# Kernel tuning notes

Measured on AMD Instinct MI355X. Metric: run time of the kernel, lower is better.

## Reference

```python
import jax, jax.numpy as jnp
import numpy as np

N, E = 50000, 800000
F_IN, F_HID, F_OUT = 128, 128, 64


def sage_conv(x, src, dst, Wl, bl, Wr, n_nodes):
    # gather source features, scatter-mean to destination nodes
    msg = x[src]                                                # [E, F]
    agg = jax.ops.segment_sum(msg, dst, num_segments=n_nodes)   # [N, F]
    cnt = jax.ops.segment_sum(jnp.ones((src.shape[0], 1), x.dtype), dst,
                              num_segments=n_nodes)             # [N, 1]
    agg = agg / jnp.maximum(cnt, 1.0)                           # mean; isolated nodes -> 0
    return agg @ Wl + bl + x @ Wr


def setup_inputs() -> dict:
    key = jax.random.key(0)
    ks = jax.random.split(key, 12)
    x = jax.random.normal(ks[0], (N, F_IN), dtype=jnp.float32)
    edge_index = jax.random.randint(ks[1], (2, E), 0, N, dtype=jnp.int64)

    def glorot(k, shape):
        lim = float(np.sqrt(6.0 / (shape[0] + shape[1])))
        return jax.random.uniform(k, shape, jnp.float32, -lim, lim)

    dims = [(F_IN, F_HID), (F_HID, F_HID), (F_HID, F_OUT)]
    params = {}
    for i, (fi, fo) in enumerate(dims):
        params[f"Wl{i}"] = glorot(ks[2 + 3 * i], (fi, fo))
        params[f"bl{i}"] = jnp.zeros((fo,), jnp.float32)
        params[f"Wr{i}"] = glorot(ks[3 + 3 * i], (fi, fo))
    return {"x": x, "edge_index": edge_index, **params}


def reference(x, edge_index, Wl0, bl0, Wr0, Wl1, bl1, Wr1, Wl2, bl2, Wr2):
    src, dst = edge_index[0], edge_index[1]
    layers = [(Wl0, bl0, Wr0), (Wl1, bl1, Wr1), (Wl2, bl2, Wr2)]
    h = x
    for i, (Wl, bl, Wr) in enumerate(layers):
        h = sage_conv(h, src, dst, Wl, bl, Wr, N)
        if i < len(layers) - 1:
            h = jax.nn.elu(h)  # dropout is identity in eval mode
    return jax.nn.log_softmax(h, axis=1)
```

## Files before the change

kernel.cpp:

```cpp
#include <hip/hip_runtime.h>
#include <hip/hip_bf16.h>

#define NN 50000
#define NE 800000
#define NPAD 50048
#define NBK 512
#define RNG 98
#define BCAP 2560
#define CSTRIDE 16
#define EPB 4096
#define NFB ((NE + EPB - 1) / EPB)
#define GB (NPAD / 64)
#define GB2 (NPAD / 32)
#define CSRCAP2 768

typedef __attribute__((ext_vector_type(8))) short bf8;
typedef __attribute__((ext_vector_type(4))) float f4;
typedef __attribute__((ext_vector_type(2))) float f2v;
typedef __attribute__((ext_vector_type(4))) unsigned int u4v;
typedef __attribute__((ext_vector_type(2))) unsigned int u2v;

__device__ __forceinline__ unsigned short f2bf(float f) {
    union { float f; unsigned int u; } x; x.f = f;
    unsigned int r = x.u + 0x7fffu + ((x.u >> 16) & 1u);
    return (unsigned short)(r >> 16);
}
__device__ __forceinline__ float b2f(short s) {
    union { unsigned int u; float f; } x;
    x.u = ((unsigned int)(unsigned short)s) << 16;
    return x.f;
}
__device__ __forceinline__ unsigned char f2fp8(float v) {
    return (unsigned char)(__builtin_amdgcn_cvt_pk_fp8_f32(v, v, 0, false) & 0xff);
}
__device__ __forceinline__ void acc16_fp8(float* acc, u4v v) {
    #pragma unroll
    for (int t = 0; t < 4; ++t) {
        f2v lo = __builtin_amdgcn_cvt_pk_f32_fp8((int)v[t], false);
        f2v hi = __builtin_amdgcn_cvt_pk_f32_fp8((int)v[t], true);
        acc[t * 4 + 0] += lo.x; acc[t * 4 + 1] += lo.y;
        acc[t * 4 + 2] += hi.x; acc[t * 4 + 3] += hi.y;
    }
}
__device__ __forceinline__ void acc8_fp8(float* acc, u2v v) {
    #pragma unroll
    for (int t = 0; t < 2; ++t) {
        f2v lo = __builtin_amdgcn_cvt_pk_f32_fp8((int)v[t], false);
        f2v hi = __builtin_amdgcn_cvt_pk_f32_fp8((int)v[t], true);
        acc[t * 4 + 0] += lo.x; acc[t * 4 + 1] += lo.y;
        acc[t * 4 + 2] += hi.x; acc[t * 4 + 3] += hi.y;
    }
}

__global__ void zero_k(int* __restrict__ cursor, int* __restrict__ rowptr) {
    cursor[threadIdx.x * CSTRIDE] = 0;
    if (threadIdx.x == 0) rowptr[NN] = NE;
}

__global__ __launch_bounds__(256) void prep_k(const int* __restrict__ ei,
                                              int* __restrict__ cursor,
                                              unsigned int* __restrict__ bucket,
                                              const float* __restrict__ Wl0, const float* __restrict__ Wr0,
                                              const float* __restrict__ Wl1, const float* __restrict__ Wr1,
                                              const float* __restrict__ Wl2, const float* __restrict__ Wr2,
                                              unsigned short* __restrict__ Bp) {
    __shared__ unsigned int sorted[EPB];
    __shared__ unsigned short sbuck[EPB];
    __shared__ int hist[NBK], ofs[NBK], gpos[NBK], stmp[256];
    const int tid = threadIdx.x;
    if (blockIdx.x >= NFB) {
        int idx = (blockIdx.x - NFB) * 256 + tid;
        const float *Wl, *Wr;
        int Mo, local;
        unsigned short* out;
        if (idx < 32768)       { Wl = Wl0; Wr = Wr0; Mo = 128; out = Bp;         local = idx; }
        else if (idx < 65536)  { Wl = Wl1; Wr = Wr1; Mo = 128; out = Bp + 32768; local = idx - 32768; }
        else if (idx < 81920)  { Wl = Wl2; Wr = Wr2; Mo = 64;  out = Bp + 65536; local = idx - 65536; }
        else return;
        int ncol = 2 * Mo;
        int k = local / ncol, c = local % ncol;
        float v = (c < Mo) ? Wl[k * Mo + c] : Wr[k * Mo + (c - Mo)];
        int cf = c >> 4, ks = k >> 5;
        int lane = (c & 15) | (((k & 31) >> 3) << 4);
        int i = k & 7;
        out[(((cf << 2) | ks) * 64 + lane) * 8 + i] = f2bf(v);
        return;
    }
    const int e0 = blockIdx.x * EPB;
    const int n = (NE - e0) < EPB ? (NE - e0) : EPB;

    for (int i = tid; i < NBK; i += 256) hist[i] = 0;
    __syncthreads();

    unsigned int ent[EPB / 256];
    short bks[EPB / 256];
    #pragma unroll
    for (int j = 0; j < EPB / 256; ++j) {
        const int li = tid + j * 256;
        int b = -1; unsigned v = 0;
        if (li < n) {
            const int e = e0 + li;
            const int s = ei[e];
            const int d = ei[NE + e];
            b = d / RNG;
            v = (unsigned)s | ((unsigned)(d - b * RNG) << 16);
            atomicAdd(&hist[b], 1);
        }
        ent[j] = v; bks[j] = (short)b;
    }
    __syncthreads();

    const int p0 = hist[2 * tid], p1 = hist[2 * tid + 1];
    stmp[tid] = p0 + p1;
    __syncthreads();
    #pragma unroll
    for (int off = 1; off < 256; off <<= 1) {
        const int t = (tid >= off) ? stmp[tid - off] : 0;
        __syncthreads();
        stmp[tid] += t;
        __syncthreads();
    }
    const int pbase = stmp[tid] - p0 - p1;
    ofs[2 * tid] = pbase;
    ofs[2 * tid + 1] = pbase + p0;
    __syncthreads();

    for (int i = tid; i < NBK; i += 256) {
        const int c = hist[i];
        gpos[i] = c ? atomicAdd(&cursor[i * CSTRIDE], c) : 0;
    }
    for (int i = tid; i < NBK; i += 256) hist[i] = ofs[i];
    __syncthreads();
    #pragma unroll
    for (int j = 0; j < EPB / 256; ++j) {
        if (bks[j] >= 0) {
            const int r = atomicAdd(&hist[(int)bks[j]], 1);
            sorted[r] = ent[j];
            sbuck[r] = (unsigned short)bks[j];
        }
    }
    __syncthreads();
    for (int i = tid; i < n; i += 256) {
        const int b = sbuck[i];
        const int idx = gpos[b] + (i - ofs[b]);
        if (idx < BCAP) bucket[(size_t)b * BCAP + idx] = sorted[i];
    }
}

__global__ __launch_bounds__(256) void mid_k(const unsigned int* __restrict__ bucket,
                                             const int* __restrict__ cursor,
                                             int* __restrict__ rowptr, int* __restrict__ csr,
                                             const float* __restrict__ x,
                                             const unsigned short* __restrict__ Bp,
                                             unsigned char* __restrict__ Yq,
                                             unsigned short* __restrict__ Z) {
    __shared__ unsigned int ent[BCAP];
    __shared__ int hist[RNG], lcur[RNG], sofs[NBK], stmp[256];
    const int tid = threadIdx.x;
    if (blockIdx.x < NBK) {
        const int b = blockIdx.x;
        const int c0 = cursor[(2 * tid) * CSTRIDE];
        const int c1 = cursor[(2 * tid + 1) * CSTRIDE];
        stmp[tid] = c0 + c1;
        __syncthreads();
        #pragma unroll
        for (int off = 1; off < 256; off <<= 1) {
            const int t = (tid >= off) ? stmp[tid - off] : 0;
            __syncthreads();
            stmp[tid] += t;
            __syncthreads();
        }
        const int pbase = stmp[tid] - c0 - c1;
        sofs[2 * tid] = pbase;
        sofs[2 * tid + 1] = pbase + c0;
        for (int i = tid; i < RNG; i += 256) { hist[i] = 0; lcur[i] = 0; }
        __syncthreads();

        const int sz0 = cursor[b * CSTRIDE];
        const int sz = sz0 < BCAP ? sz0 : BCAP;
        const int gbase = sofs[b];
        for (int i = tid; i < sz; i += 256) {
            unsigned v = bucket[(size_t)b * BCAP + i];
            ent[i] = v;
            atomicAdd(&hist[v >> 16], 1);
        }
        __syncthreads();
        if (tid == 0) {
            int acc = 0;
            #pragma unroll 2
            for (int i = 0; i < RNG; ++i) { int c = hist[i]; hist[i] = acc; acc += c; }
        }
        __syncthreads();
        const int n0 = b * RNG;
        for (int i = tid; i < RNG; i += 256) {
            int nn = n0 + i;
            if (nn < NN) rowptr[nn] = gbase + hist[i];
        }
        for (int i = tid; i < sz; i += 256) {
            unsigned v = ent[i];
            int dloc = v >> 16;
            int r = atomicAdd(&lcur[dloc], 1);
            csr[gbase + hist[dloc] + r] = (int)(v & 0xffffu);
        }
        return;
    }
    const int wave = tid >> 6;
    const int lane = tid & 63;
    const int r0 = (blockIdx.x - NBK) * 64;

    bf8 bfr[4][4];
    const bf8* bp = reinterpret_cast<const bf8*>(Bp);
    #pragma unroll
    for (int cf = 0; cf < 4; ++cf)
        #pragma unroll
        for (int ks = 0; ks < 4; ++ks)
            bfr[cf][ks] = bp[((wave * 4 + cf) * 4 + ks) * 64 + lane];

    const int rlane = lane & 15, kc = lane >> 4;
    #pragma unroll
    for (int rf = 0; rf < 4; ++rf) {
        const int arow = r0 + rf * 16 + rlane;
        const bool ok = arow < NN;
        const float4* ap = reinterpret_cast<const float4*>(x + (size_t)arow * 128);
        bf8 afr[4];
        #pragma unroll
        for (int ks = 0; ks < 4; ++ks) {
            float4 a0 = make_float4(0.f,0.f,0.f,0.f), a1 = a0;
            if (ok) { a0 = ap[ks * 8 + kc * 2]; a1 = ap[ks * 8 + kc * 2 + 1]; }
            bf8 t;
            t[0]=(short)f2bf(a0.x); t[1]=(short)f2bf(a0.y); t[2]=(short)f2bf(a0.z); t[3]=(short)f2bf(a0.w);
            t[4]=(short)f2bf(a1.x); t[5]=(short)f2bf(a1.y); t[6]=(short)f2bf(a1.z); t[7]=(short)f2bf(a1.w);
            afr[ks] = t;
        }
        f4 acc[4];
        #pragma unroll
        for (int cf = 0; cf < 4; ++cf) acc[cf] = (f4){0.f, 0.f, 0.f, 0.f};
        #pragma unroll
        for (int ks = 0; ks < 4; ++ks)
            #pragma unroll
            for (int cf = 0; cf < 4; ++cf)
                acc[cf] = __builtin_amdgcn_mfma_f32_16x16x32_bf16(afr[ks], bfr[cf][ks], acc[cf], 0, 0, 0);
        const int orow0 = r0 + rf * 16 + (lane >> 4) * 4;
        #pragma unroll
        for (int j = 0; j < 4; ++j) {
            const int orow = orow0 + j;
            if (orow < NN) {
                #pragma unroll
                for (int cf = 0; cf < 4; ++cf) {
                    const int col = (wave * 4 + cf) * 16 + rlane;
                    const float v = acc[cf][j];
                    if (col < 128) Yq[(size_t)orow * 128 + col] = f2fp8(v);
                    else           Z[(size_t)orow * 128 + (col - 128)] = f2bf(v);
                }
            }
        }
    }
}

template<int MOUT>
__global__ __launch_bounds__(256) void fused_k(const int* __restrict__ rowptr,
                                               const int* __restrict__ csr,
                                               const unsigned char* __restrict__ Yq_in,
                                               const unsigned short* __restrict__ Z_in,
                                               const float* __restrict__ bias,
                                               const unsigned short* __restrict__ Bp,
                                               unsigned char* __restrict__ Yq_out,
                                               unsigned short* __restrict__ Z_out) {
    constexpr int CFW = 2 * MOUT / 64;
    __shared__ int lcsr[CSRCAP2];
    __shared__ unsigned short tile[32 * 128];
    const int tid = threadIdx.x;
    const int n0 = blockIdx.x * 32;
    const int nend = (n0 + 32 > NN) ? NN : (n0 + 32);
    const int beg0 = rowptr[n0];
    const int tot = rowptr[nend] - beg0;
    const bool inlds = tot <= CSRCAP2;
    if (inlds) for (int i = tid; i < tot; i += 256) lcsr[i] = csr[beg0 + i];
    __syncthreads();

    const int g = tid >> 3, l = tid & 7;
    const int node = n0 + g;
    char* tbase = reinterpret_cast<char*>(tile);
    if (node < NN) {
        const int beg = rowptr[node], end = rowptr[node + 1];
        float acc[16];
        #pragma unroll
        for (int i = 0; i < 16; ++i) acc[i] = 0.f;
        int e = beg;
        for (; e + 8 <= end; e += 8) {
            int ss[8];
            #pragma unroll
            for (int j = 0; j < 8; ++j) ss[j] = inlds ? lcsr[e + j - beg0] : csr[e + j];
            u4v u[8];
            #pragma unroll
            for (int j = 0; j < 8; ++j)
                u[j] = *reinterpret_cast<const u4v*>(Yq_in + (size_t)ss[j] * 128 + l * 16);
            #pragma unroll
            for (int j = 0; j < 8; ++j) acc16_fp8(acc, u[j]);
        }
        for (; e + 4 <= end; e += 4) {
            int ss[4];
            #pragma unroll
            for (int j = 0; j < 4; ++j) ss[j] = inlds ? lcsr[e + j - beg0] : csr[e + j];
            u4v u[4];
            #pragma unroll
            for (int j = 0; j < 4; ++j)
                u[j] = *reinterpret_cast<const u4v*>(Yq_in + (size_t)ss[j] * 128 + l * 16);
            #pragma unroll
            for (int j = 0; j < 4; ++j) acc16_fp8(acc, u[j]);
        }
        for (; e < end; ++e) {
            const int s0 = inlds ? lcsr[e - beg0] : csr[e];
            acc16_fp8(acc, *reinterpret_cast<const u4v*>(Yq_in + (size_t)s0 * 128 + l * 16));
        }
        const float invd = 1.0f / fmaxf((float)(end - beg), 1.0f);
        const bf8* zp = reinterpret_cast<const bf8*>(&Z_in[(size_t)node * 128 + l * 16]);
        const float* bp = bias + l * 16;
        #pragma unroll
        for (int c8 = 0; c8 < 2; ++c8) {
            const bf8 z = zp[c8];
            bf8 o;
            #pragma unroll
            for (int i = 0; i < 8; ++i) {
                float h = acc[c8 * 8 + i] * invd + b2f(z[i]) + bp[c8 * 8 + i];
                h = h > 0.f ? h : expf(h) - 1.f;
                o[i] = (short)f2bf(h);
            }
            const unsigned byte = (unsigned)((g * 256 + l * 32 + c8 * 16) ^ ((g & 7) << 4));
            *reinterpret_cast<bf8*>(tbase + byte) = o;
        }
    } else {
        const bf8 zz = (bf8){0,0,0,0,0,0,0,0};
        #pragma unroll
        for (int c8 = 0; c8 < 2; ++c8) {
            const unsigned byte = (unsigned)((g * 256 + l * 32 + c8 * 16) ^ ((g & 7) << 4));
            *reinterpret_cast<bf8*>(tbase + byte) = zz;
        }
    }

    const int wave = tid >> 6;
    const int lane = tid & 63;
    bf8 bfr[CFW][4];
    const bf8* bpf = reinterpret_cast<const bf8*>(Bp);
    #pragma unroll
    for (int cf = 0; cf < CFW; ++cf)
        #pragma unroll
        for (int ks = 0; ks < 4; ++ks)
            bfr[cf][ks] = bpf[((wave * CFW + cf) * 4 + ks) * 64 + lane];
    __syncthreads();

    const int rlane = lane & 15, kc = lane >> 4;
    #pragma unroll
    for (int rf = 0; rf < 2; ++rf) {
        const int row = rf * 16 + rlane;
        bf8 afr[4];
        #pragma unroll
        for (int ks = 0; ks < 4; ++ks) {
            const unsigned byte = (unsigned)((row * 256 + ks * 64 + kc * 16) ^ ((row & 7) << 4));
            afr[ks] = *reinterpret_cast<const bf8*>(tbase + byte);
        }
        f4 acc[CFW];
        #pragma unroll
        for (int cf = 0; cf < CFW; ++cf) acc[cf] = (f4){0.f, 0.f, 0.f, 0.f};
        #pragma unroll
        for (int ks = 0; ks < 4; ++ks)
            #pragma unroll
            for (int cf = 0; cf < CFW; ++cf)
                acc[cf] = __builtin_amdgcn_mfma_f32_16x16x32_bf16(afr[ks], bfr[cf][ks], acc[cf], 0, 0, 0);
        const int orow0 = n0 + rf * 16 + (lane >> 4) * 4;
        #pragma unroll
        for (int j = 0; j < 4; ++j) {
            const int orow = orow0 + j;
            if (orow < NN) {
                #pragma unroll
                for (int cf = 0; cf < CFW; ++cf) {
                    const int col = (wave * CFW + cf) * 16 + rlane;
                    const float v = acc[cf][j];
                    if (col < MOUT) Yq_out[(size_t)orow * MOUT + col] = f2fp8(v);
                    else            Z_out[(size_t)orow * MOUT + (col - MOUT)] = f2bf(v);
                }
            }
        }
    }
}

__global__ __launch_bounds__(256) void gathlsm_k(const int* __restrict__ rowptr,
                                                 const int* __restrict__ csr,
                                                 const unsigned char* __restrict__ Yq2,
                                                 const unsigned short* __restrict__ Z2,
                                                 const float* __restrict__ bias,
                                                 float* __restrict__ lout) {
    __shared__ int lcsr[CSRCAP2];
    const int tid = threadIdx.x;
    const int n0 = blockIdx.x * 32;
    const int nend = (n0 + 32 > NN) ? NN : (n0 + 32);
    const int beg0 = rowptr[n0];
    const int tot = rowptr[nend] - beg0;
    const bool inlds = tot <= CSRCAP2;
    if (inlds) for (int i = tid; i < tot; i += 256) lcsr[i] = csr[beg0 + i];
    __syncthreads();

    const int g = tid >> 3, l = tid & 7;
    const int n = n0 + g;
    if (n >= NN) return;
    const int beg = rowptr[n], end = rowptr[n + 1];

    float acc[8];
    #pragma unroll
    for (int i = 0; i < 8; ++i) acc[i] = 0.f;
    int e = beg;
    for (; e + 8 <= end; e += 8) {
        int ss[8];
        #pragma unroll
        for (int j = 0; j < 8; ++j) ss[j] = inlds ? lcsr[e + j - beg0] : csr[e + j];
        u2v u[8];
        #pragma unroll
        for (int j = 0; j < 8; ++j)
            u[j] = *reinterpret_cast<const u2v*>(Yq2 + (size_t)ss[j] * 64 + l * 8);
        #pragma unroll
        for (int j = 0; j < 8; ++j) acc8_fp8(acc, u[j]);
    }
    for (; e < end; ++e) {
        const int s0 = inlds ? lcsr[e - beg0] : csr[e];
        acc8_fp8(acc, *reinterpret_cast<const u2v*>(Yq2 + (size_t)s0 * 64 + l * 8));
    }
    const float inv = 1.0f / fmaxf((float)(end - beg), 1.0f);
    const bf8 z = *reinterpret_cast<const bf8*>(&Z2[(size_t)n * 64 + l * 8]);
    float h[8];
    #pragma unroll
    for (int i = 0; i < 8; ++i) h[i] = acc[i] * inv + b2f(z[i]) + bias[l * 8 + i];

    float m = h[0];
    #pragma unroll
    for (int i = 1; i < 8; ++i) m = fmaxf(m, h[i]);
    m = fmaxf(m, __shfl_xor(m, 1, 64));
    m = fmaxf(m, __shfl_xor(m, 2, 64));
    m = fmaxf(m, __shfl_xor(m, 4, 64));
    float s = 0.f;
    #pragma unroll
    for (int i = 0; i < 8; ++i) s += expf(h[i] - m);
    s += __shfl_xor(s, 1, 64);
    s += __shfl_xor(s, 2, 64);
    s += __shfl_xor(s, 4, 64);
    const float lg = m + logf(s);
    float* op = &lout[(size_t)n * 64 + l * 8];
    float4 o0, o1;
    o0.x = h[0] - lg; o0.y = h[1] - lg; o0.z = h[2] - lg; o0.w = h[3] - lg;
    o1.x = h[4] - lg; o1.y = h[5] - lg; o1.z = h[6] - lg; o1.w = h[7] - lg;
    *reinterpret_cast<float4*>(op) = o0;
    *reinterpret_cast<float4*>(op + 4) = o1;
}

extern "C" void kernel_launch(void* const* d_in, const int* in_sizes, int n_in,
                              void* d_out, int out_size, void* d_ws, size_t ws_size,
                              hipStream_t stream) {
    const float* x   = (const float*)d_in[0];
    const int*   ei  = (const int*)d_in[1];
    const float* Wl0 = (const float*)d_in[2];
    const float* bl0 = (const float*)d_in[3];
    const float* Wr0 = (const float*)d_in[4];
    const float* Wl1 = (const float*)d_in[5];
    const float* bl1 = (const float*)d_in[6];
    const float* Wr1 = (const float*)d_in[7];
    const float* Wl2 = (const float*)d_in[8];
    const float* bl2 = (const float*)d_in[9];
    const float* Wr2 = (const float*)d_in[10];
    float* out = (float*)d_out;

    unsigned char*  Yqa = (unsigned char*)d_ws;
    unsigned char*  Yqb = Yqa + (size_t)NPAD * 128;
    unsigned short* Za  = (unsigned short*)(Yqb + (size_t)NPAD * 128);
    unsigned short* Zb  = Za + (size_t)NPAD * 128;
    unsigned short* Bp  = Zb + (size_t)NPAD * 128;
    int* rowptr = (int*)(Bp + 81920);
    int* cursor = rowptr + (NN + 2);
    int* csr    = cursor + NBK * CSTRIDE;
    unsigned int* bucket = (unsigned int*)(csr + NE);

    zero_k<<<1, NBK, 0, stream>>>(cursor, rowptr);
    prep_k<<<NFB + 320, 256, 0, stream>>>(ei, cursor, bucket, Wl0, Wr0, Wl1, Wr1, Wl2, Wr2, Bp);
    mid_k<<<NBK + GB, 256, 0, stream>>>(bucket, cursor, rowptr, csr, x, Bp, Yqa, Za);
    fused_k<128><<<GB2, 256, 0, stream>>>(rowptr, csr, Yqa, Za, bl0, Bp + 32768, Yqb, Zb);
    fused_k<64><<<GB2, 256, 0, stream>>>(rowptr, csr, Yqb, Zb, bl1, Bp + 65536, Yqa, Za);
    gathlsm_k<<<GB2, 256, 0, stream>>>(rowptr, csr, Yqa, Za, bl2, out);
}
```

Baseline: 133.6 us.

## Sort nodes by degree within each block and pack fp8 accumulation into float2

A new small kernel computes, for each 32-node group, a permutation that orders nodes by descending in-degree. The fused and final gather kernels use it to assign node slots to thread groups, so that the nodes sharing a wavefront have similar degrees and divergence in the edge loop shrinks. The fp8 accumulators are also changed to float2 vectors so the packed conversion results can be added with packed float ops. This adds one kernel launch, an extra indirect perm load per thread, and workspace placed after the bucket buffer.

```diff
diff --git a/kernel.cpp b/kernel.cpp
--- a/kernel.cpp
+++ b/kernel.cpp
@@ -33,22 +33,18 @@
 __device__ __forceinline__ unsigned char f2fp8(float v) {
     return (unsigned char)(__builtin_amdgcn_cvt_pk_fp8_f32(v, v, 0, false) & 0xff);
 }
-__device__ __forceinline__ void acc16_fp8(float* acc, u4v v) {
+__device__ __forceinline__ void acc16_fp8(f2v* acc, u4v v) {
     #pragma unroll
     for (int t = 0; t < 4; ++t) {
-        f2v lo = __builtin_amdgcn_cvt_pk_f32_fp8((int)v[t], false);
-        f2v hi = __builtin_amdgcn_cvt_pk_f32_fp8((int)v[t], true);
-        acc[t * 4 + 0] += lo.x; acc[t * 4 + 1] += lo.y;
-        acc[t * 4 + 2] += hi.x; acc[t * 4 + 3] += hi.y;
-    }
-}
-__device__ __forceinline__ void acc8_fp8(float* acc, u2v v) {
+        acc[2 * t]     += __builtin_amdgcn_cvt_pk_f32_fp8((int)v[t], false);
+        acc[2 * t + 1] += __builtin_amdgcn_cvt_pk_f32_fp8((int)v[t], true);
+    }
+}
+__device__ __forceinline__ void acc8_fp8(f2v* acc, u2v v) {
     #pragma unroll
     for (int t = 0; t < 2; ++t) {
-        f2v lo = __builtin_amdgcn_cvt_pk_f32_fp8((int)v[t], false);
-        f2v hi = __builtin_amdgcn_cvt_pk_f32_fp8((int)v[t], true);
-        acc[t * 4 + 0] += lo.x; acc[t * 4 + 1] += lo.y;
-        acc[t * 4 + 2] += hi.x; acc[t * 4 + 3] += hi.y;
+        acc[2 * t]     += __builtin_amdgcn_cvt_pk_f32_fp8((int)v[t], false);
+        acc[2 * t + 1] += __builtin_amdgcn_cvt_pk_f32_fp8((int)v[t], true);
     }
 }
 
@@ -257,9 +253,28 @@
     }
 }
 
+__global__ __launch_bounds__(256) void perm_k(const int* __restrict__ rowptr,
+                                              int* __restrict__ perm) {
+    const int w = (int)((blockIdx.x * 256 + threadIdx.x) >> 6);
+    const int lane = threadIdx.x & 63;
+    if (w >= GB2) return;
+    const int n0 = w * 32;
+    const int i = lane & 31;
+    const int n = n0 + i;
+    const int deg = (n < NN) ? (rowptr[n + 1] - rowptr[n]) : -1;
+    int rank = 0;
+    #pragma unroll
+    for (int j = 0; j < 32; ++j) {
+        const int dj = __shfl(deg, j, 64);
+        rank += (dj > deg) || (dj == deg && j < i);
+    }
+    if (lane < 32) perm[w * 32 + rank] = i;
+}
+
 template<int MOUT>
 __global__ __launch_bounds__(256) void fused_k(const int* __restrict__ rowptr,
                                                const int* __restrict__ csr,
+                                               const int* __restrict__ perm,
                                                const unsigned char* __restrict__ Yq_in,
                                                const unsigned short* __restrict__ Z_in,
                                                const float* __restrict__ bias,
@@ -278,14 +293,15 @@
     if (inlds) for (int i = tid; i < tot; i += 256) lcsr[i] = csr[beg0 + i];
     __syncthreads();
 
-    const int g = tid >> 3, l = tid & 7;
-    const int node = n0 + g;
+    const int gp = perm[blockIdx.x * 32 + (tid >> 3)];
+    const int l = tid & 7;
+    const int node = n0 + gp;
     char* tbase = reinterpret_cast<char*>(tile);
     if (node < NN) {
         const int beg = rowptr[node], end = rowptr[node + 1];
-        float acc[16];
-        #pragma unroll
-        for (int i = 0; i < 16; ++i) acc[i] = 0.f;
+        f2v acc[8];
+        #pragma unroll
+        for (int i = 0; i < 8; ++i) acc[i] = (f2v){0.f, 0.f};
         int e = beg;
         for (; e + 8 <= end; e += 8) {
             int ss[8];
@@ -322,18 +338,19 @@
             bf8 o;
             #pragma unroll
             for (int i = 0; i < 8; ++i) {
-                float h = acc[c8 * 8 + i] * invd + b2f(z[i]) + bp[c8 * 8 + i];
+                const int k = c8 * 8 + i;
+                float h = acc[k >> 1][k & 1] * invd + b2f(z[i]) + bp[c8 * 8 + i];
                 h = h > 0.f ? h : expf(h) - 1.f;
                 o[i] = (short)f2bf(h);
             }
-            const unsigned byte = (unsigned)((g * 256 + l * 32 + c8 * 16) ^ ((g & 7) << 4));
+            const unsigned byte = (unsigned)((gp * 256 + l * 32 + c8 * 16) ^ ((gp & 7) << 4));
             *reinterpret_cast<bf8*>(tbase + byte) = o;
         }
     } else {
         const bf8 zz = (bf8){0,0,0,0,0,0,0,0};
         #pragma unroll
         for (int c8 = 0; c8 < 2; ++c8) {
-            const unsigned byte = (unsigned)((g * 256 + l * 32 + c8 * 16) ^ ((g & 7) << 4));
+            const unsigned byte = (unsigned)((gp * 256 + l * 32 + c8 * 16) ^ ((gp & 7) << 4));
             *reinterpret_cast<bf8*>(tbase + byte) = zz;
         }
     }
@@ -386,6 +403,7 @@
 
 __global__ __launch_bounds__(256) void gathlsm_k(const int* __restrict__ rowptr,
                                                  const int* __restrict__ csr,
+                                                 const int* __restrict__ perm,
                                                  const unsigned char* __restrict__ Yq2,
                                                  const unsigned short* __restrict__ Z2,
                                                  const float* __restrict__ bias,
@@ -400,14 +418,15 @@
     if (inlds) for (int i = tid; i < tot; i += 256) lcsr[i] = csr[beg0 + i];
     __syncthreads();
 
-    const int g = tid >> 3, l = tid & 7;
-    const int n = n0 + g;
+    const int gp = perm[blockIdx.x * 32 + (tid >> 3)];
+    const int l = tid & 7;
+    const int n = n0 + gp;
     if (n >= NN) return;
     const int beg = rowptr[n], end = rowptr[n + 1];
 
-    float acc[8];
-    #pragma unroll
-    for (int i = 0; i < 8; ++i) acc[i] = 0.f;
+    f2v acc[4];
+    #pragma unroll
+    for (int i = 0; i < 4; ++i) acc[i] = (f2v){0.f, 0.f};
     int e = beg;
     for (; e + 8 <= end; e += 8) {
         int ss[8];
@@ -428,7 +447,7 @@
     const bf8 z = *reinterpret_cast<const bf8*>(&Z2[(size_t)n * 64 + l * 8]);
     float h[8];
     #pragma unroll
-    for (int i = 0; i < 8; ++i) h[i] = acc[i] * inv + b2f(z[i]) + bias[l * 8 + i];
+    for (int i = 0; i < 8; ++i) h[i] = acc[i >> 1][i & 1] * inv + b2f(z[i]) + bias[l * 8 + i];
 
     float m = h[0];
     #pragma unroll
@@ -476,11 +495,13 @@
     int* cursor = rowptr + (NN + 2);
     int* csr    = cursor + NBK * CSTRIDE;
     unsigned int* bucket = (unsigned int*)(csr + NE);
+    int* perm   = (int*)(bucket + (size_t)NBK * BCAP);
 
     zero_k<<<1, NBK, 0, stream>>>(cursor, rowptr);
     prep_k<<<NFB + 320, 256, 0, stream>>>(ei, cursor, bucket, Wl0, Wr0, Wl1, Wr1, Wl2, Wr2, Bp);
     mid_k<<<NBK + GB, 256, 0, stream>>>(bucket, cursor, rowptr, csr, x, Bp, Yqa, Za);
-    fused_k<128><<<GB2, 256, 0, stream>>>(rowptr, csr, Yqa, Za, bl0, Bp + 32768, Yqb, Zb);
-    fused_k<64><<<GB2, 256, 0, stream>>>(rowptr, csr, Yqb, Zb, bl1, Bp + 65536, Yqa, Za);
-    gathlsm_k<<<GB2, 256, 0, stream>>>(rowptr, csr, Yqa, Za, bl2, out);
-}
+    perm_k<<<(GB2 * 64 + 255) / 256, 256, 0, stream>>>(rowptr, perm);
+    fused_k<128><<<GB2, 256, 0, stream>>>(rowptr, csr, perm, Yqa, Za, bl0, Bp + 32768, Yqb, Zb);
+    fused_k<64><<<GB2, 256, 0, stream>>>(rowptr, csr, perm, Yqb, Zb, bl1, Bp + 65536, Yqa, Za);
+    gathlsm_k<<<GB2, 256, 0, stream>>>(rowptr, csr, perm, Yqa, Za, bl2, out);
+}
```

Measured after the change: 125.1 us. -6.4%, faster.

## Balance edge gather across lanes with merge-path chunks and LDS atomic accumulation

Applied to the files above, without the earlier changes.

Replaces per-node gather loops in the fused layer kernel and the final log-softmax kernel with an edge-balanced split. Each 8-lane group takes an equal slice of the block's edges, accumulates partial sums across node boundaries, and flushes them to a shared-memory float accumulator with atomics. The aim is to remove load imbalance from uneven node degrees within a block. The cost is LDS atomics, an extra zeroing pass and barriers, and more shared memory, which may reduce occupancy. The fp8 accumulate helpers also switch to packed float2 adds.

```diff
diff --git a/kernel.cpp b/kernel.cpp
--- a/kernel.cpp
+++ b/kernel.cpp
@@ -33,22 +33,18 @@
 __device__ __forceinline__ unsigned char f2fp8(float v) {
     return (unsigned char)(__builtin_amdgcn_cvt_pk_fp8_f32(v, v, 0, false) & 0xff);
 }
-__device__ __forceinline__ void acc16_fp8(float* acc, u4v v) {
+__device__ __forceinline__ void acc16_fp8(f2v* acc, u4v v) {
     #pragma unroll
     for (int t = 0; t < 4; ++t) {
-        f2v lo = __builtin_amdgcn_cvt_pk_f32_fp8((int)v[t], false);
-        f2v hi = __builtin_amdgcn_cvt_pk_f32_fp8((int)v[t], true);
-        acc[t * 4 + 0] += lo.x; acc[t * 4 + 1] += lo.y;
-        acc[t * 4 + 2] += hi.x; acc[t * 4 + 3] += hi.y;
-    }
-}
-__device__ __forceinline__ void acc8_fp8(float* acc, u2v v) {
+        acc[2 * t]     += __builtin_amdgcn_cvt_pk_f32_fp8((int)v[t], false);
+        acc[2 * t + 1] += __builtin_amdgcn_cvt_pk_f32_fp8((int)v[t], true);
+    }
+}
+__device__ __forceinline__ void acc8_fp8(f2v* acc, u2v v) {
     #pragma unroll
     for (int t = 0; t < 2; ++t) {
-        f2v lo = __builtin_amdgcn_cvt_pk_f32_fp8((int)v[t], false);
-        f2v hi = __builtin_amdgcn_cvt_pk_f32_fp8((int)v[t], true);
-        acc[t * 4 + 0] += lo.x; acc[t * 4 + 1] += lo.y;
-        acc[t * 4 + 2] += hi.x; acc[t * 4 + 3] += hi.y;
+        acc[2 * t]     += __builtin_amdgcn_cvt_pk_f32_fp8((int)v[t], false);
+        acc[2 * t + 1] += __builtin_amdgcn_cvt_pk_f32_fp8((int)v[t], true);
     }
 }
 
@@ -268,73 +264,106 @@
                                                unsigned short* __restrict__ Z_out) {
     constexpr int CFW = 2 * MOUT / 64;
     __shared__ int lcsr[CSRCAP2];
+    __shared__ int endsx[33];
+    __shared__ float accf[32 * 128];
     __shared__ unsigned short tile[32 * 128];
     const int tid = threadIdx.x;
     const int n0 = blockIdx.x * 32;
-    const int nend = (n0 + 32 > NN) ? NN : (n0 + 32);
-    const int beg0 = rowptr[n0];
-    const int tot = rowptr[nend] - beg0;
+    const int beg0 = rowptr[n0 < NN ? n0 : NN];
+    if (tid < 33) {
+        const int nn = n0 + tid;
+        endsx[tid] = rowptr[nn < NN ? nn : NN] - beg0;
+    }
+    float4* az = reinterpret_cast<float4*>(accf);
+    #pragma unroll
+    for (int j = 0; j < 4; ++j) az[tid + j * 256] = make_float4(0.f, 0.f, 0.f, 0.f);
+    __syncthreads();
+    const int tot = endsx[32];
     const bool inlds = tot <= CSRCAP2;
     if (inlds) for (int i = tid; i < tot; i += 256) lcsr[i] = csr[beg0 + i];
     __syncthreads();
 
-    const int g = tid >> 3, l = tid & 7;
-    const int node = n0 + g;
-    char* tbase = reinterpret_cast<char*>(tile);
-    if (node < NN) {
-        const int beg = rowptr[node], end = rowptr[node + 1];
-        float acc[16];
-        #pragma unroll
-        for (int i = 0; i < 16; ++i) acc[i] = 0.f;
-        int e = beg;
-        for (; e + 8 <= end; e += 8) {
-            int ss[8];
+    const int gid = tid >> 3, l = tid & 7;
+    {
+        const int chunk = (tot + 31) >> 5;
+        const int e_lo = min(gid * chunk, tot);
+        const int e_hi = min(e_lo + chunk, tot);
+        if (e_lo < e_hi) {
+            int cur = 0;
+            while (endsx[cur + 1] <= e_lo) ++cur;
+            f2v acc[8];
             #pragma unroll
-            for (int j = 0; j < 8; ++j) ss[j] = inlds ? lcsr[e + j - beg0] : csr[e + j];
-            u4v u[8];
+            for (int i = 0; i < 8; ++i) acc[i] = (f2v){0.f, 0.f};
+            bool dirty = false;
+            auto flush = [&]() {
+                if (dirty) {
+                    float* row = &accf[cur * 128 + l * 16];
+                    #pragma unroll
+                    for (int k = 0; k < 16; ++k) atomicAdd(&row[k], acc[k >> 1][k & 1]);
+                    #pragma unroll
+                    for (int i = 0; i < 8; ++i) acc[i] = (f2v){0.f, 0.f};
+                    dirty = false;
+                }
+            };
+            int e = e_lo;
+            for (; e + 4 <= e_hi; e += 4) {
+                int ss[4];
+                #pragma unroll
+                for (int j = 0; j < 4; ++j) ss[j] = inlds ? lcsr[e + j] : csr[beg0 + e + j];
+                u4v u[4];
+                #pragma unroll
+                for (int j = 0; j < 4; ++j)
+                    u[j] = *reinterpret_cast<const u4v*>(Yq_in + (size_t)ss[j] * 128 + l * 16);
+                #pragma unroll
+                for (int j = 0; j < 4; ++j) {
+                    const int ee = e + j;
+                    while (ee >= endsx[cur + 1]) { flush(); ++cur; }
+                    acc16_fp8(acc, u[j]);
+                    dirty = true;
+                }
+            }
+            for (; e < e_hi; ++e) {
+                const int s0 = inlds ? lcsr[e] : csr[beg0 + e];
+                const u4v u = *reinterpret_cast<const u4v*>(Yq_in + (size_t)s0 * 128 + l * 16);
+                while (e >= endsx[cur + 1]) { flush(); ++cur; }
+                acc16_fp8(acc, u);
+                dirty = true;
+            }
+            flush();
+        }
+    }
+    __syncthreads();
+
+    {
+        const int g = gid;
+        const int node = n0 + g;
+        char* tbase = reinterpret_cast<char*>(tile);
+        if (node < NN) {
+            const int deg = endsx[g + 1] - endsx[g];
+            const float invd = 1.0f / fmaxf((float)deg, 1.0f);
+            const bf8* zp = reinterpret_cast<const bf8*>(&Z_in[(size_t)node * 128 + l * 16]);
+            const float* bp = bias + l * 16;
+            const float* arow = &accf[g * 128 + l * 16];
             #pragma unroll
-            for (int j = 0; j < 8; ++j)
-                u[j] = *reinterpret_cast<const u4v*>(Yq_in + (size_t)ss[j] * 128 + l * 16);
+            for (int c8 = 0; c8 < 2; ++c8) {
+                const bf8 z = zp[c8];
+                bf8 o;
+                #pragma unroll
+                for (int i = 0; i < 8; ++i) {
+                    float h = arow[c8 * 8 + i] * invd + b2f(z[i]) + bp[c8 * 8 + i];
+                    h = h > 0.f ? h : expf(h) - 1.f;
+                    o[i] = (short)f2bf(h);
+                }
+                const unsigned byte = (unsigned)((g * 256 + l * 32 + c8 * 16) ^ ((g & 7) << 4));
+                *reinterpret_cast<bf8*>(tbase + byte) = o;
+            }
+        } else {
+            const bf8 zz = (bf8){0,0,0,0,0,0,0,0};
             #pragma unroll
-            for (int j = 0; j < 8; ++j) acc16_fp8(acc, u[j]);
-        }
-        for (; e + 4 <= end; e += 4) {
-            int ss[4];
-            #pragma unroll
-            for (int j = 0; j < 4; ++j) ss[j] = inlds ? lcsr[e + j - beg0] : csr[e + j];
-            u4v u[4];
-            #pragma unroll
-            for (int j = 0; j < 4; ++j)
-                u[j] = *reinterpret_cast<const u4v*>(Yq_in + (size_t)ss[j] * 128 + l * 16);
-            #pragma unroll
-            for (int j = 0; j < 4; ++j) acc16_fp8(acc, u[j]);
-        }
-        for (; e < end; ++e) {
-            const int s0 = inlds ? lcsr[e - beg0] : csr[e];
-            acc16_fp8(acc, *reinterpret_cast<const u4v*>(Yq_in + (size_t)s0 * 128 + l * 16));
-        }
-        const float invd = 1.0f / fmaxf((float)(end - beg), 1.0f);
-        const bf8* zp = reinterpret_cast<const bf8*>(&Z_in[(size_t)node * 128 + l * 16]);
-        const float* bp = bias + l * 16;
-        #pragma unroll
-        for (int c8 = 0; c8 < 2; ++c8) {
-            const bf8 z = zp[c8];
-            bf8 o;
-            #pragma unroll
-            for (int i = 0; i < 8; ++i) {
-                float h = acc[c8 * 8 + i] * invd + b2f(z[i]) + bp[c8 * 8 + i];
-                h = h > 0.f ? h : expf(h) - 1.f;
-                o[i] = (short)f2bf(h);
-            }
-            const unsigned byte = (unsigned)((g * 256 + l * 32 + c8 * 16) ^ ((g & 7) << 4));
-            *reinterpret_cast<bf8*>(tbase + byte) = o;
-        }
-    } else {
-        const bf8 zz = (bf8){0,0,0,0,0,0,0,0};
-        #pragma unroll
-        for (int c8 = 0; c8 < 2; ++c8) {
-            const unsigned byte = (unsigned)((g * 256 + l * 32 + c8 * 16) ^ ((g & 7) << 4));
-            *reinterpret_cast<bf8*>(tbase + byte) = zz;
+            for (int c8 = 0; c8 < 2; ++c8) {
+                const unsigned byte = (unsigned)((g * 256 + l * 32 + c8 * 16) ^ ((g & 7) << 4));
+                *reinterpret_cast<bf8*>(tbase + byte) = zz;
+            }
         }
     }
 
@@ -349,6 +378,7 @@
             bfr[cf][ks] = bpf[((wave * CFW + cf) * 4 + ks) * 64 + lane];
     __syncthreads();
 
+    char* tbase = reinterpret_cast<char*>(tile);
     const int rlane = lane & 15, kc = lane >> 4;
     #pragma unroll
     for (int rf = 0; rf < 2; ++rf) {
@@ -391,44 +421,84 @@
                                                  const float* __restrict__ bias,
                                                  float* __restrict__ lout) {
     __shared__ int lcsr[CSRCAP2];
+    __shared__ int endsx[33];
+    __shared__ float accf[32 * 64];
     const int tid = threadIdx.x;
     const int n0 = blockIdx.x * 32;
-    const int nend = (n0 + 32 > NN) ? NN : (n0 + 32);
-    const int beg0 = rowptr[n0];
-    const int tot = rowptr[nend] - beg0;
+    const int beg0 = rowptr[n0 < NN ? n0 : NN];
+    if (tid < 33) {
+        const int nn = n0 + tid;
+        endsx[tid] = rowptr[nn < NN ? nn : NN] - beg0;
+    }
+    float4* az = reinterpret_cast<float4*>(accf);
+    #pragma unroll
+    for (int j = 0; j < 2; ++j) az[tid + j * 256] = make_float4(0.f, 0.f, 0.f, 0.f);
+    __syncthreads();
+    const int tot = endsx[32];
     const bool inlds = tot <= CSRCAP2;
     if (inlds) for (int i = tid; i < tot; i += 256) lcsr[i] = csr[beg0 + i];
     __syncthreads();
 
-    const int g = tid >> 3, l = tid & 7;
-    const int n = n0 + g;
+    const int gid = tid >> 3, l = tid & 7;
+    {
+        const int chunk = (tot + 31) >> 5;
+        const int e_lo = min(gid * chunk, tot);
+        const int e_hi = min(e_lo + chunk, tot);
+        if (e_lo < e_hi) {
+            int cur = 0;
+            while (endsx[cur + 1] <= e_lo) ++cur;
+            f2v acc[4];
+            #pragma unroll
+            for (int i = 0; i < 4; ++i) acc[i] = (f2v){0.f, 0.f};
+            bool dirty = false;
+            auto flush = [&]() {
+                if (dirty) {
+                    float* row = &accf[cur * 64 + l * 8];
+                    #pragma unroll
+                    for (int k = 0; k < 8; ++k) atomicAdd(&row[k], acc[k >> 1][k & 1]);
+                    #pragma unroll
+                    for (int i = 0; i < 4; ++i) acc[i] = (f2v){0.f, 0.f};
+                    dirty = false;
+                }
+            };
+            int e = e_lo;
+            for (; e + 4 <= e_hi; e += 4) {
+                int ss[4];
+                #pragma unroll
+                for (int j = 0; j < 4; ++j) ss[j] = inlds ? lcsr[e + j] : csr[beg0 + e + j];
+                u2v u[4];
+                #pragma unroll
+                for (int j = 0; j < 4; ++j)
+                    u[j] = *reinterpret_cast<const u2v*>(Yq2 + (size_t)ss[j] * 64 + l * 8);
+                #pragma unroll
+                for (int j = 0; j < 4; ++j) {
+                    const int ee = e + j;
+                    while (ee >= endsx[cur + 1]) { flush(); ++cur; }
+                    acc8_fp8(acc, u[j]);
+                    dirty = true;
+                }
+            }
+            for (; e < e_hi; ++e) {
+                const int s0 = inlds ? lcsr[e] : csr[beg0 + e];
+                const u2v u = *reinterpret_cast<const u2v*>(Yq2 + (size_t)s0 * 64 + l * 8);
+                while (e >= endsx[cur + 1]) { flush(); ++cur; }
+                acc8_fp8(acc, u);
+                dirty = true;
+            }
+            flush();
+        }
+    }
+    __syncthreads();
+
+    const int n = n0 + gid;
     if (n >= NN) return;
-    const int beg = rowptr[n], end = rowptr[n + 1];
-
-    float acc[8];
-    #pragma unroll
-    for (int i = 0; i < 8; ++i) acc[i] = 0.f;
-    int e = beg;
-    for (; e + 8 <= end; e += 8) {
-        int ss[8];
-        #pragma unroll
-        for (int j = 0; j < 8; ++j) ss[j] = inlds ? lcsr[e + j - beg0] : csr[e + j];
-        u2v u[8];
-        #pragma unroll
-        for (int j = 0; j < 8; ++j)
-            u[j] = *reinterpret_cast<const u2v*>(Yq2 + (size_t)ss[j] * 64 + l * 8);
-        #pragma unroll
-        for (int j = 0; j < 8; ++j) acc8_fp8(acc, u[j]);
-    }
-    for (; e < end; ++e) {
-        const int s0 = inlds ? lcsr[e - beg0] : csr[e];
-        acc8_fp8(acc, *reinterpret_cast<const u2v*>(Yq2 + (size_t)s0 * 64 + l * 8));
-    }
-    const float inv = 1.0f / fmaxf((float)(end - beg), 1.0f);
+    const int deg = endsx[gid + 1] - endsx[gid];
+    const float inv = 1.0f / fmaxf((float)deg, 1.0f);
     const bf8 z = *reinterpret_cast<const bf8*>(&Z2[(size_t)n * 64 + l * 8]);
+    const float* arow = &accf[gid * 64 + l * 8];
     float h[8];
     #pragma unroll
-    for (int i = 0; i < 8; ++i) h[i] = acc[i] * inv + b2f(z[i]) + bias[l * 8 + i];
+    for (int i = 0; i < 8; ++i) h[i] = arow[i] * inv + b2f(z[i]) + bias[l * 8 + i];
 
     float m = h[0];
     #pragma unroll
```

Measured after the change: 262.1 us. 96.1% more time.
